# Optimization experiments

Measured on AMD Instinct MI355X. Metric: run time of the kernel, lower is better.

The kernel has to match this reference:

```python
import jax, jax.numpy as jnp
import numpy as np

EPS = 1e-5

def _conv1x1(x, w, b):
    # x: [B, Cin, L], w: [Cout, Cin], b: [Cout]
    return jnp.einsum('oc,bcl->bol', w, x) + b[None, :, None]

def _bn(x, g, b):
    # BatchNorm1d in training mode: batch stats over (B, L), biased variance
    m = jnp.mean(x, axis=(0, 2), keepdims=True)
    v = jnp.var(x, axis=(0, 2), keepdims=True)
    return g[None, :, None] * (x - m) * jax.lax.rsqrt(v + EPS) + b[None, :, None]

def setup_inputs() -> dict:
    key = jax.random.key(0)
    ks = jax.random.split(key, 16)
    B, H, L, K = 32, 32, 32768, 7
    rel, im, out = H // 16, H // 8, H // 4          # 2, 4, 8
    cat = (1 + K) * rel                              # 16
    w = lambda k, shape: jax.random.normal(k, shape, jnp.float32) * 0.1
    return {
        'x': jax.random.normal(ks[0], (B, H, L), jnp.float32),
        'w_phi': w(ks[1], (rel, H)),  'b_phi': w(ks[2], (rel,)),
        'w_psi': w(ks[3], (rel, H)),  'b_psi': w(ks[4], (rel,)),
        'w_beta': w(ks[5], (out, H)), 'b_beta': w(ks[6], (out,)),
        'w_cw1': w(ks[7], (im, cat)), 'b_cw1': w(ks[8], (im,)),
        'w_cw2': w(ks[9], (out, im)), 'b_cw2': w(ks[10], (out,)),
        'w_out': w(ks[11], (H, out)), 'b_out': w(ks[12], (H,)),
        'g_cat': jnp.ones((cat,), jnp.float32),  'be_cat': jnp.zeros((cat,), jnp.float32),
        'g_im': jnp.ones((im,), jnp.float32),    'be_im': jnp.zeros((im,), jnp.float32),
        'g_aggr': jnp.ones((out,), jnp.float32), 'be_aggr': jnp.zeros((out,), jnp.float32),
        'g_hid': jnp.ones((H,), jnp.float32),    'be_hid': jnp.zeros((H,), jnp.float32),
        'kernel_size': 7,
    }

def reference(x, w_phi, b_phi, w_psi, b_psi, w_beta, b_beta,
              w_cw1, b_cw1, w_cw2, b_cw2, w_out, b_out,
              g_cat, be_cat, g_im, be_im, g_aggr, be_aggr, g_hid, be_hid,
              kernel_size):
    B, H, L = x.shape
    phi = _conv1x1(x, w_phi, b_phi)                       # [B, rel, L]
    psi = _conv1x1(x, w_psi, b_psi)                       # [B, rel, L]
    p = kernel_size // 2
    psi_pad = jnp.pad(psi, ((0, 0), (0, 0), (p, p)))
    # F.unfold with kernel (k,1): channel index = c*k + j -> stack kernel axis after channel
    psi_unf = jnp.stack([psi_pad[:, :, j:j + L] for j in range(kernel_size)], axis=2)
    psi_unf = psi_unf.reshape(B, psi.shape[1] * kernel_size, L)   # [B, rel*k, L]
    h = jnp.concatenate([phi, psi_unf], axis=1)           # [B, (1+k)*rel, L]
    h = jax.nn.relu(_bn(h, g_cat, be_cat))
    h = _conv1x1(h, w_cw1, b_cw1)
    h = jax.nn.relu(_bn(h, g_im, be_im))
    weight = _conv1x1(h, w_cw2, b_cw2)                    # [B, out, L]
    beta = _conv1x1(x, w_beta, b_beta)                    # [B, out, L]
    aggr = jax.nn.relu(_bn(weight * beta, g_aggr, be_aggr))
    y = x + _conv1x1(aggr, w_out, b_out)
    return jax.nn.relu(_bn(y, g_hid, be_hid))
```

## Files before the change

### kernel.cpp

```cpp
#include <hip/hip_runtime.h>
#include <math.h>

#define Bn 32
#define Hc 32
#define Ln 32768
#define RELC 2
#define IMC 4
#define OC 8
#define CATC 16
#define KS 7
#define NPOS (Bn*Ln)
#define TPB 256
#define VPT 4
#define PPB (TPB*VPT)
#define TILES (Ln/PPB)
#define NBLK (Bn*TILES)
#define NSLOT 16
#define SSTR 128

#define iS_PHI  0
#define iSS_PHI 2
#define iS_PSI  4
#define iSS_PSI 6
#define iS_T    8
#define iSS_T   12
#define iS_AP   16
#define iSS_AP  24
#define iS_Y    32
#define iSS_Y   64
#define bPF  0
#define bPFS 6
#define bQL  12
#define bQLS 18
#define NBST 24

#define FMA4(A,S,V) { A.x=fmaf((S),(V).x,A.x); A.y=fmaf((S),(V).y,A.y); A.z=fmaf((S),(V).z,A.z); A.w=fmaf((S),(V).w,A.w); }

__device__ inline float4 affrelu(float4 v, float a, float d){
    float4 r;
    r.x=fmaxf(fmaf(a,v.x,d),0.f); r.y=fmaxf(fmaf(a,v.y,d),0.f);
    r.z=fmaxf(fmaf(a,v.z,d),0.f); r.w=fmaxf(fmaf(a,v.w,d),0.f);
    return r;
}
__device__ inline double wredd(double v){
    #pragma unroll
    for (int o=32;o>0;o>>=1) v += __shfl_down(v,o,64);
    return v;
}
__device__ inline float wredf(float v){
    #pragma unroll
    for (int o=32;o>0;o>>=1) v += __shfl_down(v,o,64);
    return v;
}
__device__ inline void atomAddD(double* p, double v){ unsafeAtomicAdd(p, v); }

__device__ inline unsigned short f2b(float f){
    unsigned int u = __float_as_uint(f);
    u += 0x7FFFu + ((u>>16)&1u);
    return (unsigned short)(u>>16);
}
__device__ inline float b2f(unsigned short h){ return __uint_as_float(((unsigned int)h)<<16); }
__device__ inline ushort4 pack4r(float4 v, float4* r){
    ushort4 h;
    h.x=f2b(v.x); h.y=f2b(v.y); h.z=f2b(v.z); h.w=f2b(v.w);
    r->x=b2f(h.x); r->y=b2f(h.y); r->z=b2f(h.z); r->w=b2f(h.w);
    return h;
}
__device__ inline ushort4 pack4(float4 v){
    ushort4 h;
    h.x=f2b(v.x); h.y=f2b(v.y); h.z=f2b(v.z); h.w=f2b(v.w);
    return h;
}
__device__ inline float4 unpack4(ushort4 h){
    return make_float4(b2f(h.x),b2f(h.y),b2f(h.z),b2f(h.w));
}
typedef unsigned short us8 __attribute__((ext_vector_type(8)));
typedef unsigned short us4 __attribute__((ext_vector_type(4)));
typedef float f4nt __attribute__((ext_vector_type(4)));
__device__ inline void ntstore4(float* p, float4 v){
    union { float4 a; f4nt b; } u; u.a = v;
    __builtin_nontemporal_store(u.b, (f4nt*)p);
}
__device__ inline void ntstoreu4(unsigned short* p, ushort4 v){
    union { ushort4 a; us4 b; } u; u.a = v;
    __builtin_nontemporal_store(u.b, (us4*)p);
}

template<int NCH>
__device__ void affines(const double* __restrict__ stats, const double* __restrict__ bstats,
                        const float* g_cat, const float* be_cat,
                        const float* g_im,  const float* be_im,
                        const float* g_ag,  const float* be_ag,
                        const float* g_hid, const float* be_hid,
                        double (*redS)[16], double (*redQ)[16],
                        double* bstL, float* aAll, float* dAll, int tid)
{
    if (tid < NBST) bstL[tid] = bstats[tid];
    for (int p = tid; p < NCH*16; p += TPB){
        int ch = p >> 4, s = p & 15;
        int si, qi;
        if (ch < 2)       { si = iS_PHI+ch;           qi = iSS_PHI+ch; }
        else if (ch < 16) { int cp=(ch-2)/KS;         si = iS_PSI+cp;  qi = iSS_PSI+cp; }
        else if (ch < 20) { int i=ch-16;              si = iS_T+i;     qi = iSS_T+i; }
        else if (ch < 28) { int o=ch-20;              si = iS_AP+o;    qi = iSS_AP+o; }
        else              { int h=ch-28;              si = iS_Y+h;     qi = iSS_Y+h; }
        redS[ch][s] = stats[(size_t)s*SSTR + si];
        redQ[ch][s] = stats[(size_t)s*SSTR + qi];
    }
    __syncthreads();
    if (tid < NCH){
        double S=0, SS=0;
        #pragma unroll
        for (int s=0;s<16;++s){ S += redS[tid][s]; SS += redQ[tid][s]; }
        float g, be;
        if (tid < 16){
            if (tid >= 2){
                int cp=(tid-2)/KS, j=(tid-2)%KS, d=j-KS/2;
                if (d>0) for (int i=0;i<d;++i)   { S-=bstL[bPF+cp*3+i]; SS-=bstL[bPFS+cp*3+i]; }
                if (d<0) for (int i=3+d;i<3;++i) { S-=bstL[bQL+cp*3+i]; SS-=bstL[bQLS+cp*3+i]; }
            }
            g=g_cat[tid]; be=be_cat[tid];
        } else if (tid < 20){ g=g_im[tid-16]; be=be_im[tid-16]; }
        else if (tid < 28){ g=g_ag[tid-20]; be=be_ag[tid-20]; }
        else { g=g_hid[tid-28]; be=be_hid[tid-28]; }
        const double N=(double)NPOS;
        double m=S/N, v=SS/N-m*m, inv=1.0/sqrt(v+1e-5);
        aAll[tid]=(float)(g*inv);
        dAll[tid]=be-(float)(m*inv*g);
    }
}

__global__ void __launch_bounds__(TPB) k1m(
    const float* __restrict__ x,
    const float* __restrict__ w_phi, const float* __restrict__ b_phi,
    const float* __restrict__ w_psi, const float* __restrict__ b_psi,
    const float* __restrict__ w_beta,const float* __restrict__ b_beta,
    unsigned short* __restrict__ phiB, unsigned short* __restrict__ psiB,
    unsigned short* __restrict__ betaB, unsigned short* __restrict__ xB,
    double* __restrict__ stats, double* __restrict__ bstats)
{
    __shared__ __align__(16) float wl[Hc*12 + 12];
    __shared__ double rbuf[4][8];
    const int tid = threadIdx.x;
    for (int i = tid; i < Hc*12; i += TPB) {
        int h = i/12, j = i%12;
        float v;
        if (j < 2)      v = w_phi[j*Hc + h];
        else if (j < 4) v = w_psi[(j-2)*Hc + h];
        else            v = w_beta[(j-4)*Hc + h];
        wl[h*12 + j] = v;
    }
    if (tid < 12)
        wl[Hc*12+tid] = (tid<2) ? b_phi[tid] : (tid<4) ? b_psi[tid-2] : b_beta[tid-4];
    __syncthreads();

    const int b    = blockIdx.x / TILES;
    const int tile = blockIdx.x % TILES;
    const int l0   = tile*PPB + tid*VPT;
    double* st = stats + (size_t)(blockIdx.x & (NSLOT-1))*SSTR;

    float4 acc[12];
    #pragma unroll
    for (int j=0;j<12;++j){ float bb = wl[Hc*12+j]; acc[j]=make_float4(bb,bb,bb,bb); }

    const float* xp = x + (size_t)b*Hc*Ln + l0;
    unsigned short* xw = xB + (size_t)b*Hc*Ln + l0;
    #pragma unroll 8
    for (int h=0; h<Hc; ++h) {
        const float4 xv = *(const float4*)(xp + (size_t)h*Ln);
        const float4 w0 = *(const float4*)(&wl[h*12+0]);
        const float4 w1 = *(const float4*)(&wl[h*12+4]);
        const float4 w2 = *(const float4*)(&wl[h*12+8]);
        FMA4(acc[0],w0.x,xv); FMA4(acc[1],w0.y,xv); FMA4(acc[2],w0.z,xv); FMA4(acc[3],w0.w,xv);
        FMA4(acc[4],w1.x,xv); FMA4(acc[5],w1.y,xv); FMA4(acc[6],w1.z,xv); FMA4(acc[7],w1.w,xv);
        FMA4(acc[8],w2.x,xv); FMA4(acc[9],w2.y,xv); FMA4(acc[10],w2.z,xv); FMA4(acc[11],w2.w,xv);
        ntstoreu4(xw + (size_t)h*Ln, pack4(xv));
    }

    float4 rphi[2], rpsi[2];
    #pragma unroll
    for (int c=0;c<RELC;++c){
        ushort4 hp = pack4r(acc[c], &rphi[c]);
        ntstoreu4(phiB + ((size_t)(b*RELC+c))*Ln + l0, hp);
        ushort4 hq = pack4r(acc[2+c], &rpsi[c]);
        ntstoreu4(psiB + ((size_t)(b*RELC+c))*Ln + l0, hq);
    }
    #pragma unroll
    for (int o=0;o<OC;++o)
        ntstoreu4(betaB + ((size_t)(b*OC+o))*Ln + l0, pack4(acc[4+o]));

    double vals[8];
    #pragma unroll
    for (int c=0;c<2;++c){
        float4 v = rphi[c];
        vals[c]   = (double)v.x+v.y+v.z+v.w;
        vals[2+c] = (double)v.x*v.x+(double)v.y*v.y+(double)v.z*v.z+(double)v.w*v.w;
        float4 u = rpsi[c];
        vals[4+c] = (double)u.x+u.y+u.z+u.w;
        vals[6+c] = (double)u.x*u.x+(double)u.y*u.y+(double)u.z*u.z+(double)u.w*u.w;
    }
    if (tile==0 || tile==TILES-1) {
        #pragma unroll
        for (int c=0;c<2;++c){
            const float pv[4] = {rpsi[c].x, rpsi[c].y, rpsi[c].z, rpsi[c].w};
            #pragma unroll
            for (int e=0;e<4;++e){
                int le = l0+e;
                if (le < 3) {
                    atomAddD(&bstats[bPF +c*3+le], (double)pv[e]);
                    atomAddD(&bstats[bPFS+c*3+le], (double)pv[e]*pv[e]);
                }
                if (le >= Ln-3) {
                    int i = le-(Ln-3);
                    atomAddD(&bstats[bQL +c*3+i], (double)pv[e]);
                    atomAddD(&bstats[bQLS+c*3+i], (double)pv[e]*pv[e]);
                }
            }
        }
    }
    const int lane=tid&63, wid=tid>>6;
    #pragma unroll
    for (int i=0;i<8;++i){ double r=wredd(vals[i]); if(lane==0) rbuf[wid][i]=r; }
    __syncthreads();
    if (tid<8) atomAddD(&st[iS_PHI+tid], rbuf[0][tid]+rbuf[1][tid]+rbuf[2][tid]+rbuf[3][tid]);
}

#define STAGE_PSI_V(psiT)                                                                  \
    {                                                                                      \
        int c_ = tid >> 7, k_ = tid & 127;                                                 \
        us8 v_ = *(const us8*)(psiB + ((size_t)(b*RELC+c_))*Ln + lb + 8*k_);               \
        _Pragma("unroll")                                                                  \
        for (int j_=0;j_<8;++j_) psiT[c_][3+8*k_+j_] = b2f(v_[j_]);                        \
        if (tid < 6){ int cc=tid/3, ii=tid%3;                                              \
            psiT[cc][ii] = (tile>0) ? b2f(psiB[((size_t)(b*RELC+cc))*Ln + lb-3+ii]) : 0.f; }\
        else if (tid < 12){ int kk=tid-6, cc=kk/3, ii=kk%3;                                \
            psiT[cc][1027+ii] = (tile<TILES-1) ? b2f(psiB[((size_t)(b*RELC+cc))*Ln + lb+1024+ii]) : 0.f; } \
    }

#define COMPUTE_T(tacc,aCat,dCat,w1s,b1s,psiT)                                             \
    _Pragma("unroll")                                                                      \
    for (int o=0;o<IMC;++o){ float bb=b1s[o]; tacc[o]=make_float4(bb,bb,bb,bb); }          \
    _Pragma("unroll")                                                                      \
    for (int c=0;c<RELC;++c){                                                              \
        float4 pv = unpack4(*(const ushort4*)(phiB + ((size_t)(b*RELC+c))*Ln + lb + li));  \
        float4 hv = affrelu(pv, aCat[c], dCat[c]);                                         \
        _Pragma("unroll")                                                                  \
        for (int o=0;o<IMC;++o) FMA4(tacc[o], w1s[o*CATC+c], hv);                          \
    }                                                                                      \
    _Pragma("unroll")                                                                      \
    for (int c=0;c<RELC;++c){                                                              \
        float4 A  = *(const float4*)&psiT[c][li];                                          \
        float4 Bv = *(const float4*)&psiT[c][li+4];                                        \
        float4 Cv = *(const float4*)&psiT[c][li+8];                                        \
        float pr[12] = {A.x,A.y,A.z,A.w, Bv.x,Bv.y,Bv.z,Bv.w, Cv.x,Cv.y,Cv.z,Cv.w};        \
        _Pragma("unroll")                                                                  \
        for (int j=0;j<KS;++j){                                                            \
            int ch = 2 + c*KS + j;                                                         \
            float a=aCat[ch], d=dCat[ch];                                                  \
            float4 hv;                                                                     \
            hv.x=fmaxf(fmaf(a,pr[j+0],d),0.f);                                             \
            hv.y=fmaxf(fmaf(a,pr[j+1],d),0.f);                                             \
            hv.z=fmaxf(fmaf(a,pr[j+2],d),0.f);                                             \
            hv.w=fmaxf(fmaf(a,pr[j+3],d),0.f);                                             \
            _Pragma("unroll")                                                              \
            for (int o=0;o<IMC;++o) FMA4(tacc[o], w1s[o*CATC+ch], hv);                     \
        }                                                                                  \
    }

#define COMPUTE_AG(ag,tacc,aIm,dIm,aAg,dAg,w2s,b2s)                                        \
    {                                                                                      \
        float4 h2[IMC];                                                                    \
        _Pragma("unroll")                                                                  \
        for (int i=0;i<IMC;++i) h2[i]=affrelu(tacc[i],aIm[i],dIm[i]);                      \
        _Pragma("unroll")                                                                  \
        for (int o=0;o<OC;++o){                                                            \
            float bb=b2s[o];                                                               \
            float4 w=make_float4(bb,bb,bb,bb);                                             \
            _Pragma("unroll")                                                              \
            for (int i=0;i<IMC;++i) FMA4(w,w2s[o*IMC+i],h2[i]);                            \
            float4 bv = unpack4(*(const ushort4*)(betaB + ((size_t)(b*OC+o))*Ln + lb + li)); \
            float4 av; av.x=w.x*bv.x; av.y=w.y*bv.y; av.z=w.z*bv.z; av.w=w.w*bv.w;         \
            ag[o]=affrelu(av, aAg[o], dAg[o]);                                             \
        }                                                                                  \
    }

__global__ void __launch_bounds__(TPB) k3t(
    const unsigned short* __restrict__ phiB, const unsigned short* __restrict__ psiB,
    const float* __restrict__ w_cw1, const float* __restrict__ b_cw1,
    const float* __restrict__ g_cat, const float* __restrict__ be_cat,
    double* __restrict__ stats, const double* __restrict__ bstats)
{
    __shared__ float w1s[IMC*CATC], b1s[IMC];
    __shared__ __align__(16) float psiT[2][1032];
    __shared__ double rbuf[4][8];
    __shared__ double redS[16][16], redQ[16][16];
    __shared__ double bstL[NBST];
    __shared__ float aAll[16], dAll[16];
    const int tid = threadIdx.x;
    const int b    = blockIdx.x / TILES;
    const int tile = blockIdx.x % TILES;
    const int lb   = tile*PPB;
    const int li   = tid*VPT;
    double* st = stats + (size_t)(blockIdx.x & (NSLOT-1))*SSTR;

    if (tid < IMC*CATC) w1s[tid] = w_cw1[tid];
    if (tid < IMC)      b1s[tid] = b_cw1[tid];
    STAGE_PSI_V(psiT)
    affines<16>(stats,bstats, g_cat,be_cat, 0,0, 0,0, 0,0, redS,redQ,bstL,aAll,dAll, tid);
    __syncthreads();

    float4 tacc[IMC];
    COMPUTE_T(tacc,aAll,dAll,w1s,b1s,psiT)

    double vals[8];
    #pragma unroll
    for (int o=0;o<IMC;++o){
        float4 v = tacc[o];
        vals[o]   = (double)v.x+v.y+v.z+v.w;
        vals[4+o] = (double)v.x*v.x+(double)v.y*v.y+(double)v.z*v.z+(double)v.w*v.w;
    }
    const int lane=tid&63, wid=tid>>6;
    #pragma unroll
    for (int i=0;i<8;++i){ double r=wredd(vals[i]); if(lane==0) rbuf[wid][i]=r; }
    __syncthreads();
    if (tid<8) atomAddD(&st[iS_T+tid], rbuf[0][tid]+rbuf[1][tid]+rbuf[2][tid]+rbuf[3][tid]);
}

__global__ void __launch_bounds__(TPB) k5a(
    const unsigned short* __restrict__ phiB, const unsigned short* __restrict__ psiB,
    const unsigned short* __restrict__ betaB,
    const float* __restrict__ w_cw1, const float* __restrict__ b_cw1,
    const float* __restrict__ w_cw2, const float* __restrict__ b_cw2,
    const float* __restrict__ g_cat, const float* __restrict__ be_cat,
    const float* __restrict__ g_im,  const float* __restrict__ be_im,
    double* __restrict__ stats, const double* __restrict__ bstats)
{
    __shared__ float w1s[IMC*CATC], b1s[IMC], w2s[OC*IMC], b2s[OC];
    __shared__ __align__(16) float psiT[2][1032];
    __shared__ double rbuf[4][16];
    __shared__ double redS[20][16], redQ[20][16];
    __shared__ double bstL[NBST];
    __shared__ float aAll[20], dAll[20];
    const int tid = threadIdx.x;
    const int b    = blockIdx.x / TILES;
    const int tile = blockIdx.x % TILES;
    const int lb   = tile*PPB;
    const int li   = tid*VPT;
    double* st = stats + (size_t)(blockIdx.x & (NSLOT-1))*SSTR;

    if (tid < IMC*CATC) w1s[tid] = w_cw1[tid];
    if (tid < IMC)      b1s[tid] = b_cw1[tid];
    if (tid>=64 && tid<64+OC*IMC) w2s[tid-64]=w_cw2[tid-64];
    if (tid>=96 && tid<96+OC)     b2s[tid-96]=b_cw2[tid-96];
    STAGE_PSI_V(psiT)
    affines<20>(stats,bstats, g_cat,be_cat, g_im,be_im, 0,0, 0,0, redS,redQ,bstL,aAll,dAll, tid);
    __syncthreads();

    float4 tacc[IMC];
    COMPUTE_T(tacc,aAll,dAll,w1s,b1s,psiT)

    double vals[16];
    {
        float4 h2[IMC];
        #pragma unroll
        for (int i=0;i<IMC;++i) h2[i]=affrelu(tacc[i],aAll[16+i],dAll[16+i]);
        #pragma unroll
        for (int o=0;o<OC;++o){
            float bb=b2s[o];
            float4 w=make_float4(bb,bb,bb,bb);
            #pragma unroll
            for (int i=0;i<IMC;++i) FMA4(w,w2s[o*IMC+i],h2[i]);
            float4 bv = unpack4(*(const ushort4*)(betaB + ((size_t)(b*OC+o))*Ln + lb + li));
            float4 av; av.x=w.x*bv.x; av.y=w.y*bv.y; av.z=w.z*bv.z; av.w=w.w*bv.w;
            vals[o]   = (double)av.x+av.y+av.z+av.w;
            vals[8+o] = (double)av.x*av.x+(double)av.y*av.y+(double)av.z*av.z+(double)av.w*av.w;
        }
    }
    const int lane=tid&63, wid=tid>>6;
    #pragma unroll
    for (int i=0;i<16;++i){ double r=wredd(vals[i]); if(lane==0) rbuf[wid][i]=r; }
    __syncthreads();
    if (tid<16) atomAddD(&st[iS_AP+tid], rbuf[0][tid]+rbuf[1][tid]+rbuf[2][tid]+rbuf[3][tid]);
}

__global__ void __launch_bounds__(TPB) k7y(
    const unsigned short* __restrict__ xB,
    const unsigned short* __restrict__ phiB, const unsigned short* __restrict__ psiB,
    const unsigned short* __restrict__ betaB,
    const float* __restrict__ w_cw1, const float* __restrict__ b_cw1,
    const float* __restrict__ w_cw2, const float* __restrict__ b_cw2,
    const float* __restrict__ w_out, const float* __restrict__ b_out,
    const float* __restrict__ g_cat, const float* __restrict__ be_cat,
    const float* __restrict__ g_im,  const float* __restrict__ be_im,
    const float* __restrict__ g_ag,  const float* __restrict__ be_ag,
    double* __restrict__ stats, const double* __restrict__ bstats)
{
    __shared__ float w1s[IMC*CATC], b1s[IMC], w2s[OC*IMC], b2s[OC];
    __shared__ __align__(16) float wos[Hc*OC];
    __shared__ float bos[Hc];
    __shared__ __align__(16) float psiT[2][1032];
    __shared__ float fredS[Hc][4], fredQ[Hc][4];
    __shared__ double redS[28][16], redQ[28][16];
    __shared__ double bstL[NBST];
    __shared__ float aAll[28], dAll[28];
    const int tid = threadIdx.x;
    const int b    = blockIdx.x / TILES;
    const int tile = blockIdx.x % TILES;
    const int lb   = tile*PPB;
    const int li   = tid*VPT;
    double* st = stats + (size_t)(blockIdx.x & (NSLOT-1))*SSTR;

    if (tid < IMC*CATC) w1s[tid] = w_cw1[tid];
    if (tid < IMC)      b1s[tid] = b_cw1[tid];
    if (tid>=64 && tid<64+OC*IMC) w2s[tid-64]=w_cw2[tid-64];
    if (tid>=96 && tid<96+OC)     b2s[tid-96]=b_cw2[tid-96];
    wos[tid] = w_out[tid];
    if (tid>=128 && tid<128+Hc) bos[tid-128]=b_out[tid-128];
    STAGE_PSI_V(psiT)
    affines<28>(stats,bstats, g_cat,be_cat, g_im,be_im, g_ag,be_ag, 0,0,
                redS,redQ,bstL,aAll,dAll, tid);
    __syncthreads();

    float4 tacc[IMC];
    COMPUTE_T(tacc,aAll,dAll,w1s,b1s,psiT)
    float4 ag[OC];
    COMPUTE_AG(ag,tacc,(aAll+16),(dAll+16),(aAll+20),(dAll+20),w2s,b2s)

    const int lane=tid&63, wid=tid>>6;
    const unsigned short* xb = xB + (size_t)b*Hc*Ln + lb + li;
    #pragma unroll 8
    for (int h=0;h<Hc;++h){
        float4 y = unpack4(*(const ushort4*)(xb + (size_t)h*Ln));
        float bb=bos[h]; y.x+=bb; y.y+=bb; y.z+=bb; y.w+=bb;
        #pragma unroll
        for (int o=0;o<OC;++o) FMA4(y, wos[h*OC+o], ag[o]);
        float fs=y.x+y.y+y.z+y.w;
        float fq=y.x*y.x+y.y*y.y+y.z*y.z+y.w*y.w;
        fs=wredf(fs); fq=wredf(fq);
        if (lane==0){ fredS[h][wid]=fs; fredQ[h][wid]=fq; }
    }
    __syncthreads();
    if (tid<Hc){
        double s=(double)fredS[tid][0]+fredS[tid][1]+fredS[tid][2]+fredS[tid][3];
        double q=(double)fredQ[tid][0]+fredQ[tid][1]+fredQ[tid][2]+fredQ[tid][3];
        atomAddD(&st[iS_Y +tid], s);
        atomAddD(&st[iSS_Y+tid], q);
    }
}

__global__ void __launch_bounds__(TPB) k9o(
    const unsigned short* __restrict__ xB,
    const unsigned short* __restrict__ phiB, const unsigned short* __restrict__ psiB,
    const unsigned short* __restrict__ betaB,
    const float* __restrict__ w_cw1, const float* __restrict__ b_cw1,
    const float* __restrict__ w_cw2, const float* __restrict__ b_cw2,
    const float* __restrict__ w_out, const float* __restrict__ b_out,
    const float* __restrict__ g_cat, const float* __restrict__ be_cat,
    const float* __restrict__ g_im,  const float* __restrict__ be_im,
    const float* __restrict__ g_ag,  const float* __restrict__ be_ag,
    const float* __restrict__ g_hid, const float* __restrict__ be_hid,
    float* __restrict__ out,
    const double* __restrict__ stats, const double* __restrict__ bstats)
{
    __shared__ float w1s[IMC*CATC], b1s[IMC], w2s[OC*IMC], b2s[OC];
    __shared__ __align__(16) float wos[Hc*OC];
    __shared__ float bos[Hc];
    __shared__ __align__(16) float psiT[2][1032];
    __shared__ double redS[60][16], redQ[60][16];
    __shared__ double bstL[NBST];
    __shared__ float aAll[60], dAll[60];
    const int tid = threadIdx.x;
    const int b    = blockIdx.x / TILES;
    const int tile = blockIdx.x % TILES;
    const int lb   = tile*PPB;
    const int li   = tid*VPT;

    if (tid < IMC*CATC) w1s[tid] = w_cw1[tid];
    if (tid < IMC)      b1s[tid] = b_cw1[tid];
    if (tid>=64 && tid<64+OC*IMC) w2s[tid-64]=w_cw2[tid-64];
    if (tid>=96 && tid<96+OC)     b2s[tid-96]=b_cw2[tid-96];
    wos[tid] = w_out[tid];
    if (tid>=128 && tid<128+Hc) bos[tid-128]=b_out[tid-128];
    STAGE_PSI_V(psiT)
    affines<60>(stats,bstats, g_cat,be_cat, g_im,be_im, g_ag,be_ag, g_hid,be_hid,
                redS,redQ,bstL,aAll,dAll, tid);
    __syncthreads();

    float4 tacc[IMC];
    COMPUTE_T(tacc,aAll,dAll,w1s,b1s,psiT)
    float4 ag[OC];
    COMPUTE_AG(ag,tacc,(aAll+16),(dAll+16),(aAll+20),(dAll+20),w2s,b2s)

    const unsigned short* xb = xB + (size_t)b*Hc*Ln + lb + li;
    float* ob = out + (size_t)b*Hc*Ln + lb + li;
    #pragma unroll 8
    for (int h=0;h<Hc;++h){
        float4 y = unpack4(*(const ushort4*)(xb + (size_t)h*Ln));
        float bb=bos[h]; y.x+=bb; y.y+=bb; y.z+=bb; y.w+=bb;
        #pragma unroll
        for (int o=0;o<OC;++o) FMA4(y, wos[h*OC+o], ag[o]);
        ntstore4(ob + (size_t)h*Ln, affrelu(y, aAll[28+h], dAll[28+h]));
    }
}

extern "C" void kernel_launch(void* const* d_in, const int* in_sizes, int n_in,
                              void* d_out, int out_size, void* d_ws, size_t ws_size,
                              hipStream_t stream)
{
    const float* x     =(const float*)d_in[0];
    const float* w_phi =(const float*)d_in[1];  const float* b_phi =(const float*)d_in[2];
    const float* w_psi =(const float*)d_in[3];  const float* b_psi =(const float*)d_in[4];
    const float* w_beta=(const float*)d_in[5];  const float* b_beta=(const float*)d_in[6];
    const float* w_cw1 =(const float*)d_in[7];  const float* b_cw1 =(const float*)d_in[8];
    const float* w_cw2 =(const float*)d_in[9];  const float* b_cw2 =(const float*)d_in[10];
    const float* w_out =(const float*)d_in[11]; const float* b_out =(const float*)d_in[12];
    const float* g_cat =(const float*)d_in[13]; const float* be_cat=(const float*)d_in[14];
    const float* g_im  =(const float*)d_in[15]; const float* be_im =(const float*)d_in[16];
    const float* g_ag  =(const float*)d_in[17]; const float* be_ag =(const float*)d_in[18];
    const float* g_hid =(const float*)d_in[19]; const float* be_hid=(const float*)d_in[20];

    double* stats  = (double*)d_ws;
    double* bstats = stats + (size_t)NSLOT*SSTR;
    unsigned short* base = (unsigned short*)((char*)d_ws + 32768);
    unsigned short* phiB  = base;
    unsigned short* psiB  = phiB  + (size_t)Bn*RELC*Ln;
    unsigned short* betaB = psiB  + (size_t)Bn*RELC*Ln;
    unsigned short* xB    = betaB + (size_t)Bn*OC*Ln;

    hipMemsetAsync(d_ws, 0, ((size_t)NSLOT*SSTR + NBST)*sizeof(double), stream);
    k1m<<<NBLK, TPB, 0, stream>>>(x, w_phi,b_phi, w_psi,b_psi, w_beta,b_beta,
                                  phiB,psiB,betaB,xB, stats,bstats);
    k3t<<<NBLK, TPB, 0, stream>>>(phiB,psiB, w_cw1,b_cw1, g_cat,be_cat, stats,bstats);
    k5a<<<NBLK, TPB, 0, stream>>>(phiB,psiB,betaB, w_cw1,b_cw1, w_cw2,b_cw2,
                                  g_cat,be_cat, g_im,be_im, stats,bstats);
    k7y<<<NBLK, TPB, 0, stream>>>(xB, phiB,psiB,betaB, w_cw1,b_cw1, w_cw2,b_cw2, w_out,b_out,
                                  g_cat,be_cat, g_im,be_im, g_ag,be_ag, stats,bstats);
    k9o<<<NBLK, TPB, 0, stream>>>(xB, phiB,psiB,betaB, w_cw1,b_cw1, w_cw2,b_cw2, w_out,b_out,
                                  g_cat,be_cat, g_im,be_im, g_ag,be_ag, g_hid,be_hid,
                                  (float*)d_out, stats,bstats);
}
```

Baseline: 173.2 us.

## Store intermediates in tile-contiguous chunked layout with separate x conversion pass

Adds a new kernel that converts x to bf16 and writes it into a tile-major chunked layout, so each block's data for all channels is contiguous. All intermediate buffers (phi, psi, beta, x copy) move to this per-block layout, and their stores become regular instead of nontemporal. The goal is contiguous per-block memory access in the downstream kernels. In exchange it adds an extra launch and makes the first pass read x from the bf16 copy rather than fusing the conversion. That means an extra round trip of the bf16 x copy through memory.

```diff
diff --git a/kernel.cpp b/kernel.cpp
--- a/kernel.cpp
+++ b/kernel.cpp
@@ -17,6 +17,9 @@
 #define NBLK (Bn*TILES)
 #define NSLOT 16
 #define SSTR 128
+#define PCH (RELC*PPB)
+#define BCH (OC*PPB)
+#define XCH (Hc*PPB)
 
 #define iS_PHI  0
 #define iSS_PHI 2
@@ -75,15 +78,10 @@
     return make_float4(b2f(h.x),b2f(h.y),b2f(h.z),b2f(h.w));
 }
 typedef unsigned short us8 __attribute__((ext_vector_type(8)));
-typedef unsigned short us4 __attribute__((ext_vector_type(4)));
 typedef float f4nt __attribute__((ext_vector_type(4)));
 __device__ inline void ntstore4(float* p, float4 v){
     union { float4 a; f4nt b; } u; u.a = v;
     __builtin_nontemporal_store(u.b, (f4nt*)p);
-}
-__device__ inline void ntstoreu4(unsigned short* p, ushort4 v){
-    union { ushort4 a; us4 b; } u; u.a = v;
-    __builtin_nontemporal_store(u.b, (us4*)p);
 }
 
 template<int NCH>
@@ -130,13 +128,27 @@
     }
 }
 
-__global__ void __launch_bounds__(TPB) k1m(
-    const float* __restrict__ x,
+__global__ void __launch_bounds__(TPB) k0(const float* __restrict__ x, unsigned short* __restrict__ xC)
+{
+    const int r = blockIdx.x;
+    const int b = r >> 5, h = r & 31;
+    const float* src = x + (size_t)r*Ln;
+    unsigned short* dstBase = xC + (size_t)b*TILES*XCH + (size_t)h*PPB + threadIdx.x*4;
+    const float* s4 = src + threadIdx.x*4;
+    #pragma unroll 4
+    for (int t = 0; t < TILES; ++t){
+        float4 v = *(const float4*)(s4 + (size_t)t*PPB);
+        *(ushort4*)(dstBase + (size_t)t*XCH) = pack4(v);
+    }
+}
+
+__global__ void __launch_bounds__(TPB) k1c(
+    const unsigned short* __restrict__ xC,
     const float* __restrict__ w_phi, const float* __restrict__ b_phi,
     const float* __restrict__ w_psi, const float* __restrict__ b_psi,
     const float* __restrict__ w_beta,const float* __restrict__ b_beta,
-    unsigned short* __restrict__ phiB, unsigned short* __restrict__ psiB,
-    unsigned short* __restrict__ betaB, unsigned short* __restrict__ xB,
+    unsigned short* __restrict__ phiC, unsigned short* __restrict__ psiC,
+    unsigned short* __restrict__ betaC,
     double* __restrict__ stats, double* __restrict__ bstats)
 {
     __shared__ __align__(16) float wl[Hc*12 + 12];
@@ -154,40 +166,37 @@
         wl[Hc*12+tid] = (tid<2) ? b_phi[tid] : (tid<4) ? b_psi[tid-2] : b_beta[tid-4];
     __syncthreads();
 
-    const int b    = blockIdx.x / TILES;
-    const int tile = blockIdx.x % TILES;
-    const int l0   = tile*PPB + tid*VPT;
-    double* st = stats + (size_t)(blockIdx.x & (NSLOT-1))*SSTR;
+    const int cidx = blockIdx.x;
+    const int tile = cidx % TILES;
+    const int li   = tid*VPT;
+    double* st = stats + (size_t)(cidx & (NSLOT-1))*SSTR;
 
     float4 acc[12];
     #pragma unroll
     for (int j=0;j<12;++j){ float bb = wl[Hc*12+j]; acc[j]=make_float4(bb,bb,bb,bb); }
 
-    const float* xp = x + (size_t)b*Hc*Ln + l0;
-    unsigned short* xw = xB + (size_t)b*Hc*Ln + l0;
+    const unsigned short* xb = xC + (size_t)cidx*XCH + li;
     #pragma unroll 8
     for (int h=0; h<Hc; ++h) {
-        const float4 xv = *(const float4*)(xp + (size_t)h*Ln);
+        const float4 xv = unpack4(*(const ushort4*)(xb + (size_t)h*PPB));
         const float4 w0 = *(const float4*)(&wl[h*12+0]);
         const float4 w1 = *(const float4*)(&wl[h*12+4]);
         const float4 w2 = *(const float4*)(&wl[h*12+8]);
         FMA4(acc[0],w0.x,xv); FMA4(acc[1],w0.y,xv); FMA4(acc[2],w0.z,xv); FMA4(acc[3],w0.w,xv);
         FMA4(acc[4],w1.x,xv); FMA4(acc[5],w1.y,xv); FMA4(acc[6],w1.z,xv); FMA4(acc[7],w1.w,xv);
         FMA4(acc[8],w2.x,xv); FMA4(acc[9],w2.y,xv); FMA4(acc[10],w2.z,xv); FMA4(acc[11],w2.w,xv);
-        ntstoreu4(xw + (size_t)h*Ln, pack4(xv));
-    }
-
+    }
     float4 rphi[2], rpsi[2];
     #pragma unroll
     for (int c=0;c<RELC;++c){
         ushort4 hp = pack4r(acc[c], &rphi[c]);
-        ntstoreu4(phiB + ((size_t)(b*RELC+c))*Ln + l0, hp);
+        *(ushort4*)(phiC + (size_t)cidx*PCH + c*PPB + li) = hp;
         ushort4 hq = pack4r(acc[2+c], &rpsi[c]);
-        ntstoreu4(psiB + ((size_t)(b*RELC+c))*Ln + l0, hq);
+        *(ushort4*)(psiC + (size_t)cidx*PCH + c*PPB + li) = hq;
     }
     #pragma unroll
     for (int o=0;o<OC;++o)
-        ntstoreu4(betaB + ((size_t)(b*OC+o))*Ln + l0, pack4(acc[4+o]));
+        *(ushort4*)(betaC + (size_t)cidx*BCH + o*PPB + li) = pack4(acc[4+o]);
 
     double vals[8];
     #pragma unroll
@@ -205,7 +214,7 @@
             const float pv[4] = {rpsi[c].x, rpsi[c].y, rpsi[c].z, rpsi[c].w};
             #pragma unroll
             for (int e=0;e<4;++e){
-                int le = l0+e;
+                int le = tile*PPB + li + e;
                 if (le < 3) {
                     atomAddD(&bstats[bPF +c*3+le], (double)pv[e]);
                     atomAddD(&bstats[bPFS+c*3+le], (double)pv[e]*pv[e]);
@@ -228,13 +237,13 @@
 #define STAGE_PSI_V(psiT)                                                                  \
     {                                                                                      \
         int c_ = tid >> 7, k_ = tid & 127;                                                 \
-        us8 v_ = *(const us8*)(psiB + ((size_t)(b*RELC+c_))*Ln + lb + 8*k_);               \
+        us8 v_ = *(const us8*)(psiC + (size_t)cidx*PCH + c_*PPB + 8*k_);                   \
         _Pragma("unroll")                                                                  \
         for (int j_=0;j_<8;++j_) psiT[c_][3+8*k_+j_] = b2f(v_[j_]);                        \
         if (tid < 6){ int cc=tid/3, ii=tid%3;                                              \
-            psiT[cc][ii] = (tile>0) ? b2f(psiB[((size_t)(b*RELC+cc))*Ln + lb-3+ii]) : 0.f; }\
+            psiT[cc][ii] = (tile>0) ? b2f(psiC[(size_t)(cidx-1)*PCH + cc*PPB + 1021+ii]) : 0.f; }\
         else if (tid < 12){ int kk=tid-6, cc=kk/3, ii=kk%3;                                \
-            psiT[cc][1027+ii] = (tile<TILES-1) ? b2f(psiB[((size_t)(b*RELC+cc))*Ln + lb+1024+ii]) : 0.f; } \
+            psiT[cc][1027+ii] = (tile<TILES-1) ? b2f(psiC[(size_t)(cidx+1)*PCH + cc*PPB + ii]) : 0.f; } \
     }
 
 #define COMPUTE_T(tacc,aCat,dCat,w1s,b1s,psiT)                                             \
@@ -242,7 +251,7 @@
     for (int o=0;o<IMC;++o){ float bb=b1s[o]; tacc[o]=make_float4(bb,bb,bb,bb); }          \
     _Pragma("unroll")                                                                      \
     for (int c=0;c<RELC;++c){                                                              \
-        float4 pv = unpack4(*(const ushort4*)(phiB + ((size_t)(b*RELC+c))*Ln + lb + li));  \
+        float4 pv = unpack4(*(const ushort4*)(phiC + (size_t)cidx*PCH + c*PPB + li));      \
         float4 hv = affrelu(pv, aCat[c], dCat[c]);                                         \
         _Pragma("unroll")                                                                  \
         for (int o=0;o<IMC;++o) FMA4(tacc[o], w1s[o*CATC+c], hv);                          \
@@ -278,14 +287,14 @@
             float4 w=make_float4(bb,bb,bb,bb);                                             \
             _Pragma("unroll")                                                              \
             for (int i=0;i<IMC;++i) FMA4(w,w2s[o*IMC+i],h2[i]);                            \
-            float4 bv = unpack4(*(const ushort4*)(betaB + ((size_t)(b*OC+o))*Ln + lb + li)); \
+            float4 bv = unpack4(*(const ushort4*)(betaC + (size_t)cidx*BCH + o*PPB + li)); \
             float4 av; av.x=w.x*bv.x; av.y=w.y*bv.y; av.z=w.z*bv.z; av.w=w.w*bv.w;         \
             ag[o]=affrelu(av, aAg[o], dAg[o]);                                             \
         }                                                                                  \
     }
 
 __global__ void __launch_bounds__(TPB) k3t(
-    const unsigned short* __restrict__ phiB, const unsigned short* __restrict__ psiB,
+    const unsigned short* __restrict__ phiC, const unsigned short* __restrict__ psiC,
     const float* __restrict__ w_cw1, const float* __restrict__ b_cw1,
     const float* __restrict__ g_cat, const float* __restrict__ be_cat,
     double* __restrict__ stats, const double* __restrict__ bstats)
@@ -297,11 +306,10 @@
     __shared__ double bstL[NBST];
     __shared__ float aAll[16], dAll[16];
     const int tid = threadIdx.x;
-    const int b    = blockIdx.x / TILES;
-    const int tile = blockIdx.x % TILES;
-    const int lb   = tile*PPB;
+    const int cidx = blockIdx.x;
+    const int tile = cidx % TILES;
     const int li   = tid*VPT;
-    double* st = stats + (size_t)(blockIdx.x & (NSLOT-1))*SSTR;
+    double* st = stats + (size_t)(cidx & (NSLOT-1))*SSTR;
 
     if (tid < IMC*CATC) w1s[tid] = w_cw1[tid];
     if (tid < IMC)      b1s[tid] = b_cw1[tid];
@@ -327,8 +335,8 @@
 }
 
 __global__ void __launch_bounds__(TPB) k5a(
-    const unsigned short* __restrict__ phiB, const unsigned short* __restrict__ psiB,
-    const unsigned short* __restrict__ betaB,
+    const unsigned short* __restrict__ phiC, const unsigned short* __restrict__ psiC,
+    const unsigned short* __restrict__ betaC,
     const float* __restrict__ w_cw1, const float* __restrict__ b_cw1,
     const float* __restrict__ w_cw2, const float* __restrict__ b_cw2,
     const float* __restrict__ g_cat, const float* __restrict__ be_cat,
@@ -342,11 +350,10 @@
     __shared__ double bstL[NBST];
     __shared__ float aAll[20], dAll[20];
     const int tid = threadIdx.x;
-    const int b    = blockIdx.x / TILES;
-    const int tile = blockIdx.x % TILES;
-    const int lb   = tile*PPB;
+    const int cidx = blockIdx.x;
+    const int tile = cidx % TILES;
     const int li   = tid*VPT;
-    double* st = stats + (size_t)(blockIdx.x & (NSLOT-1))*SSTR;
+    double* st = stats + (size_t)(cidx & (NSLOT-1))*SSTR;
 
     if (tid < IMC*CATC) w1s[tid] = w_cw1[tid];
     if (tid < IMC)      b1s[tid] = b_cw1[tid];
@@ -370,7 +377,7 @@
             float4 w=make_float4(bb,bb,bb,bb);
             #pragma unroll
             for (int i=0;i<IMC;++i) FMA4(w,w2s[o*IMC+i],h2[i]);
-            float4 bv = unpack4(*(const ushort4*)(betaB + ((size_t)(b*OC+o))*Ln + lb + li));
+            float4 bv = unpack4(*(const ushort4*)(betaC + (size_t)cidx*BCH + o*PPB + li));
             float4 av; av.x=w.x*bv.x; av.y=w.y*bv.y; av.z=w.z*bv.z; av.w=w.w*bv.w;
             vals[o]   = (double)av.x+av.y+av.z+av.w;
             vals[8+o] = (double)av.x*av.x+(double)av.y*av.y+(double)av.z*av.z+(double)av.w*av.w;
@@ -384,9 +391,9 @@
 }
 
 __global__ void __launch_bounds__(TPB) k7y(
-    const unsigned short* __restrict__ xB,
-    const unsigned short* __restrict__ phiB, const unsigned short* __restrict__ psiB,
-    const unsigned short* __restrict__ betaB,
+    const unsigned short* __restrict__ xC,
+    const unsigned short* __restrict__ phiC, const unsigned short* __restrict__ psiC,
+    const unsigned short* __restrict__ betaC,
     const float* __restrict__ w_cw1, const float* __restrict__ b_cw1,
     const float* __restrict__ w_cw2, const float* __restrict__ b_cw2,
     const float* __restrict__ w_out, const float* __restrict__ b_out,
@@ -404,11 +411,10 @@
     __shared__ double bstL[NBST];
     __shared__ float aAll[28], dAll[28];
     const int tid = threadIdx.x;
-    const int b    = blockIdx.x / TILES;
-    const int tile = blockIdx.x % TILES;
-    const int lb   = tile*PPB;
+    const int cidx = blockIdx.x;
+    const int tile = cidx % TILES;
     const int li   = tid*VPT;
-    double* st = stats + (size_t)(blockIdx.x & (NSLOT-1))*SSTR;
+    double* st = stats + (size_t)(cidx & (NSLOT-1))*SSTR;
 
     if (tid < IMC*CATC) w1s[tid] = w_cw1[tid];
     if (tid < IMC)      b1s[tid] = b_cw1[tid];
@@ -427,10 +433,10 @@
     COMPUTE_AG(ag,tacc,(aAll+16),(dAll+16),(aAll+20),(dAll+20),w2s,b2s)
 
     const int lane=tid&63, wid=tid>>6;
-    const unsigned short* xb = xB + (size_t)b*Hc*Ln + lb + li;
+    const unsigned short* xb = xC + (size_t)cidx*XCH + li;
     #pragma unroll 8
     for (int h=0;h<Hc;++h){
-        float4 y = unpack4(*(const ushort4*)(xb + (size_t)h*Ln));
+        float4 y = unpack4(*(const ushort4*)(xb + (size_t)h*PPB));
         float bb=bos[h]; y.x+=bb; y.y+=bb; y.z+=bb; y.w+=bb;
         #pragma unroll
         for (int o=0;o<OC;++o) FMA4(y, wos[h*OC+o], ag[o]);
@@ -449,9 +455,9 @@
 }
 
 __global__ void __launch_bounds__(TPB) k9o(
-    const unsigned short* __restrict__ xB,
-    const unsigned short* __restrict__ phiB, const unsigned short* __restrict__ psiB,
-    const unsigned short* __restrict__ betaB,
+    const unsigned short* __restrict__ xC,
+    const unsigned short* __restrict__ phiC, const unsigned short* __restrict__ psiC,
+    const unsigned short* __restrict__ betaC,
     const float* __restrict__ w_cw1, const float* __restrict__ b_cw1,
     const float* __restrict__ w_cw2, const float* __restrict__ b_cw2,
     const float* __restrict__ w_out, const float* __restrict__ b_out,
@@ -470,9 +476,9 @@
     __shared__ double bstL[NBST];
     __shared__ float aAll[60], dAll[60];
     const int tid = threadIdx.x;
-    const int b    = blockIdx.x / TILES;
-    const int tile = blockIdx.x % TILES;
-    const int lb   = tile*PPB;
+    const int cidx = blockIdx.x;
+    const int b    = cidx / TILES;
+    const int tile = cidx % TILES;
     const int li   = tid*VPT;
 
     if (tid < IMC*CATC) w1s[tid] = w_cw1[tid];
@@ -491,11 +497,11 @@
     float4 ag[OC];
     COMPUTE_AG(ag,tacc,(aAll+16),(dAll+16),(aAll+20),(dAll+20),w2s,b2s)
 
-    const unsigned short* xb = xB + (size_t)b*Hc*Ln + lb + li;
-    float* ob = out + (size_t)b*Hc*Ln + lb + li;
+    const unsigned short* xb = xC + (size_t)cidx*XCH + li;
+    float* ob = out + (size_t)b*Hc*Ln + (size_t)tile*PPB + li;
     #pragma unroll 8
     for (int h=0;h<Hc;++h){
-        float4 y = unpack4(*(const ushort4*)(xb + (size_t)h*Ln));
+        float4 y = unpack4(*(const ushort4*)(xb + (size_t)h*PPB));
         float bb=bos[h]; y.x+=bb; y.y+=bb; y.z+=bb; y.w+=bb;
         #pragma unroll
         for (int o=0;o<OC;++o) FMA4(y, wos[h*OC+o], ag[o]);
@@ -522,20 +528,21 @@
     double* stats  = (double*)d_ws;
     double* bstats = stats + (size_t)NSLOT*SSTR;
     unsigned short* base = (unsigned short*)((char*)d_ws + 32768);
-    unsigned short* phiB  = base;
-    unsigned short* psiB  = phiB  + (size_t)Bn*RELC*Ln;
-    unsigned short* betaB = psiB  + (size_t)Bn*RELC*Ln;
-    unsigned short* xB    = betaB + (size_t)Bn*OC*Ln;
+    unsigned short* phiC  = base;
+    unsigned short* psiC  = phiC  + (size_t)NBLK*PCH;
+    unsigned short* betaC = psiC  + (size_t)NBLK*PCH;
+    unsigned short* xC    = betaC + (size_t)NBLK*BCH;
 
     hipMemsetAsync(d_ws, 0, ((size_t)NSLOT*SSTR + NBST)*sizeof(double), stream);
-    k1m<<<NBLK, TPB, 0, stream>>>(x, w_phi,b_phi, w_psi,b_psi, w_beta,b_beta,
-                                  phiB,psiB,betaB,xB, stats,bstats);
-    k3t<<<NBLK, TPB, 0, stream>>>(phiB,psiB, w_cw1,b_cw1, g_cat,be_cat, stats,bstats);
-    k5a<<<NBLK, TPB, 0, stream>>>(phiB,psiB,betaB, w_cw1,b_cw1, w_cw2,b_cw2,
+    k0 <<<Bn*Hc, TPB, 0, stream>>>(x, xC);
+    k1c<<<NBLK, TPB, 0, stream>>>(xC, w_phi,b_phi, w_psi,b_psi, w_beta,b_beta,
+                                  phiC,psiC,betaC, stats,bstats);
+    k3t<<<NBLK, TPB, 0, stream>>>(phiC,psiC, w_cw1,b_cw1, g_cat,be_cat, stats,bstats);
+    k5a<<<NBLK, TPB, 0, stream>>>(phiC,psiC,betaC, w_cw1,b_cw1, w_cw2,b_cw2,
                                   g_cat,be_cat, g_im,be_im, stats,bstats);
-    k7y<<<NBLK, TPB, 0, stream>>>(xB, phiB,psiB,betaB, w_cw1,b_cw1, w_cw2,b_cw2, w_out,b_out,
+    k7y<<<NBLK, TPB, 0, stream>>>(xC, phiC,psiC,betaC, w_cw1,b_cw1, w_cw2,b_cw2, w_out,b_out,
                                   g_cat,be_cat, g_im,be_im, g_ag,be_ag, stats,bstats);
-    k9o<<<NBLK, TPB, 0, stream>>>(xB, phiB,psiB,betaB, w_cw1,b_cw1, w_cw2,b_cw2, w_out,b_out,
+    k9o<<<NBLK, TPB, 0, stream>>>(xC, phiC,psiC,betaC, w_cw1,b_cw1, w_cw2,b_cw2, w_out,b_out,
                                   g_cat,be_cat, g_im,be_im, g_ag,be_ag, g_hid,be_hid,
                                   (float*)d_out, stats,bstats);
 }
```

Result: faster. 167.3 us (-3.4%).
